# Performance work log

Hardware: AMD Instinct MI355X
Metric: run time of the kernel (lower is better)

Reference implementation:

```python
import jax, jax.numpy as jnp
import numpy as np

NODE = 100000
REL = 2000
E = 600000  # n_edges == triple_size
D = 128
DEPTH = 2
HEADS = 1


def setup_inputs() -> dict:
    key = jax.random.key(0)
    ks = jax.random.split(key, 8)
    features = jax.random.normal(ks[0], (NODE, D), jnp.float32)
    rel_emb = jax.random.normal(ks[1], (REL, D), jnp.float32)
    sp_val = jax.random.uniform(ks[2], (E,), jnp.float32)
    attn_kernels = jax.random.normal(ks[3], (DEPTH, HEADS, 3 * D), jnp.float32) * 0.1
    adj_src = jnp.sort(jax.random.randint(ks[4], (E,), 0, NODE))  # tf.segment_sum needs sorted ids
    adj_dst = jax.random.randint(ks[5], (E,), 0, NODE)
    sp_rel = jax.random.randint(ks[6], (E,), 0, REL)
    sp_row = jnp.arange(E)  # sparse (triple, rel) matrix row indices
    return dict(features=features, rel_emb=rel_emb, sp_val=sp_val,
                attn_kernels=attn_kernels, adj_src=adj_src, adj_dst=adj_dst,
                sp_rel=sp_rel, sp_row=sp_row)


def _segment_softmax(logits, seg, num):
    m = jax.ops.segment_max(logits, seg, num_segments=num)
    e = jnp.exp(logits - m[seg])
    s = jax.ops.segment_sum(e, seg, num_segments=num)
    return e / s[seg]


def reference(features, rel_emb, sp_val, attn_kernels, adj_src, adj_dst, sp_rel, sp_row):
    act = jax.nn.relu
    feats = act(features)
    outputs = [feats]
    for l in range(DEPTH):
        heads = []
        for h in range(HEADS):
            ak = attn_kernels[l, h]  # [3D]
            # sparse (triple x rel) @ rel_emb -> per-edge relation embedding [E, D]
            rels = jax.ops.segment_sum(sp_val[:, None] * rel_emb[sp_rel], sp_row,
                                       num_segments=E)
            # tf.nn.l2_normalize with eps 1e-12
            rels = rels * jax.lax.rsqrt(jnp.maximum(jnp.sum(rels * rels, axis=1,
                                                            keepdims=True), 1e-12))
            neighs = feats[adj_dst]  # [E, D]
            selfs = feats[adj_src]   # [E, D]
            # Householder-style reflection of neighbor features across rels
            proj = jnp.sum(neighs * rels, axis=1, keepdims=True) * rels
            neighs = neighs - 2.0 * proj
            # attention logits: concat([selfs, neighs, rels]) @ ak
            att = selfs @ ak[:D] + neighs @ ak[D:2 * D] + rels @ ak[2 * D:]
            a = _segment_softmax(att, adj_src, NODE)  # tf.sparse_softmax per row
            heads.append(jax.ops.segment_sum(neighs * a[:, None], adj_src,
                                             num_segments=NODE))
        feats = heads[0] if HEADS == 1 else jnp.concatenate(heads, axis=1)
        feats = act(feats)
        outputs.append(feats)
    return jnp.concatenate(outputs, axis=1)  # [NODE, D*(DEPTH+1)]
```

## Files before the change

kernel.cpp:

```cpp
#include <hip/hip_runtime.h>
#include <math.h>
#include <stdint.h>

#define NNODE 100000
#define NREL 2000
#define NEDGE 600000
#define DIM 128
#define OUTC 384
#define LOG2E 1.4426950408889634f

#define RELU_BLOCKS 12500
#define PRE_BLOCKS 500
#define ROW_BLOCKS ((NNODE + 1 + 255) / 256)

typedef float f32x2 __attribute__((ext_vector_type(2)));

__device__ __forceinline__ float wave_sum(float v) {
#pragma unroll
    for (int off = 32; off > 0; off >>= 1)
        v += __shfl_xor(v, off, 64);
    return v;
}

__device__ __forceinline__ float dpp_sum16(float x) {
    x += __int_as_float(__builtin_amdgcn_mov_dpp(__float_as_int(x), 0xB1, 0xF, 0xF, true));
    x += __int_as_float(__builtin_amdgcn_mov_dpp(__float_as_int(x), 0x4E, 0xF, 0xF, true));
    x += __int_as_float(__builtin_amdgcn_mov_dpp(__float_as_int(x), 0x124, 0xF, 0xF, true));
    x += __int_as_float(__builtin_amdgcn_mov_dpp(__float_as_int(x), 0x128, 0xF, 0xF, true));
    return x;
}

__device__ __forceinline__ unsigned short f2bf(float f) {
    unsigned b = __float_as_uint(f);
    return (unsigned short)((b + 0x7fffu + ((b >> 16) & 1u)) >> 16);
}
__device__ __forceinline__ unsigned pack2(float f0, float f1) {
    return (unsigned)f2bf(f0) | ((unsigned)f2bf(f1) << 16);
}
__device__ __forceinline__ f32x2 bf2(unsigned u) {
    f32x2 r;
    r.x = __uint_as_float(u << 16);
    r.y = __uint_as_float(u & 0xffff0000u);
    return r;
}

__global__ void k_setup(const float* __restrict__ f, const float* __restrict__ rel,
                        const float* __restrict__ attn, const int* __restrict__ adj_src,
                        float* __restrict__ out, unsigned short* __restrict__ fm,
                        unsigned short* __restrict__ relm,
                        float* __restrict__ relnorm2, float* __restrict__ rdB,
                        float* __restrict__ rdC,
                        float* __restrict__ nd0, int* __restrict__ row_ptr) {
    int b = blockIdx.x;
    if (b < RELU_BLOCKS) {
        int idx = b * 256 + threadIdx.x;
        int n = idx >> 5;
        int q = idx & 31;
        float4 v = reinterpret_cast<const float4*>(f + (size_t)n * DIM)[q];
        v.x = fmaxf(v.x, 0.f); v.y = fmaxf(v.y, 0.f);
        v.z = fmaxf(v.z, 0.f); v.w = fmaxf(v.w, 0.f);
        reinterpret_cast<float4*>(out + (size_t)n * OUTC)[q] = v;
        uint2 p;
        p.x = pack2(v.x, v.y);
        p.y = pack2(v.z, v.w);
        reinterpret_cast<uint2*>(fm + (size_t)n * DIM)[q] = p;
        float4 bb = reinterpret_cast<const float4*>(attn + DIM)[q];
        float pb = v.x * bb.x + v.y * bb.y + v.z * bb.z + v.w * bb.w;
#pragma unroll
        for (int off = 1; off <= 16; off <<= 1)
            pb += __shfl_xor(pb, off, 64);
        if (q == 0) nd0[n] = pb * LOG2E;
    } else if (b < RELU_BLOCKS + PRE_BLOCKS) {
        int wid = (b - RELU_BLOCKS) * 4 + (threadIdx.x >> 6);
        int lane = threadIdx.x & 63;
        float2 v = reinterpret_cast<const float2*>(rel + (size_t)wid * DIM)[lane];
        reinterpret_cast<unsigned*>(relm + (size_t)wid * DIM)[lane] = pack2(v.x, v.y);
        float2 b0 = reinterpret_cast<const float2*>(attn + DIM)[lane];
        float2 c0 = reinterpret_cast<const float2*>(attn + 2 * DIM)[lane];
        float2 b1 = reinterpret_cast<const float2*>(attn + 3 * DIM + DIM)[lane];
        float2 c1 = reinterpret_cast<const float2*>(attn + 3 * DIM + 2 * DIM)[lane];
        float n2  = wave_sum(v.x * v.x + v.y * v.y);
        float pb0 = wave_sum(v.x * b0.x + v.y * b0.y);
        float pc0 = wave_sum(v.x * c0.x + v.y * c0.y);
        float pb1 = wave_sum(v.x * b1.x + v.y * b1.y);
        float pc1 = wave_sum(v.x * c1.x + v.y * c1.y);
        if (lane == 0) {
            relnorm2[wid] = n2;
            rdB[wid] = pb0;        rdC[wid] = pc0;
            rdB[NREL + wid] = pb1; rdC[NREL + wid] = pc1;
        }
    } else {
        int n = (b - RELU_BLOCKS - PRE_BLOCKS) * 256 + threadIdx.x;
        if (n <= NNODE) {
            int lo = 0, hi = NEDGE;
            while (lo < hi) {
                int mid = (lo + hi) >> 1;
                if (adj_src[mid] < n) lo = mid + 1; else hi = mid;
            }
            row_ptr[n] = lo;
        }
    }
}

__global__ void k_edges(const float* __restrict__ sp_val, const int* __restrict__ sp_rel,
                        const int* __restrict__ adj_dst,
                        const float* __restrict__ relnorm2,
                        const float* __restrict__ rdB, const float* __restrict__ rdC,
                        const float* __restrict__ nd0,
                        float4* __restrict__ ed0, float4* __restrict__ ed1) {
    int e = blockIdx.x * blockDim.x + threadIdx.x;
    if (e >= NEDGE) return;
    float v = sp_val[e];
    int r = sp_rel[e];
    int dst = adj_dst[e];
    float n2 = relnorm2[r];
    float sc = v * rsqrtf(fmaxf(v * v * n2, 1e-12f));
    float q2 = 2.f * sc * sc;
    float scl = sc * LOG2E, q2l = q2 * LOG2E;
    unsigned pk = ((unsigned)dst << 11) | (unsigned)r;
    float pkf = __uint_as_float(pk);
    ed0[e] = make_float4(nd0[dst] + scl * rdC[r], q2l * rdB[r], q2, pkf);
    ed1[e] = make_float4(scl * rdC[NREL + r], q2l * rdB[NREL + r], q2, pkf);
}

__global__ void k_fold(float4* __restrict__ ed, const float* __restrict__ nd) {
    int e = blockIdx.x * blockDim.x + threadIdx.x;
    if (e >= NEDGE) return;
    float4 v = ed[e];
    unsigned pk = __float_as_uint(v.w);
    ed[e].x = v.x + nd[pk >> 11];
}

template<int USE_ED, int WRITE_NEXT>
__global__ __launch_bounds__(256, 8)
void k_gat(const unsigned short* __restrict__ fin_m,
           float* __restrict__ fout,
           unsigned short* __restrict__ fout_m,
           const unsigned short* __restrict__ relm,
           const float4* __restrict__ edata,
           const int* __restrict__ adj_dst, const int* __restrict__ sp_rel,
           const float* __restrict__ sp_val, const float* __restrict__ relnorm2,
           const float* __restrict__ rdB, const float* __restrict__ rdC,
           const float* __restrict__ ndpre,
           const int* __restrict__ row_ptr,
           float* __restrict__ nd_n,
           const float* __restrict__ akB_next) {
    int wv = (blockIdx.x * blockDim.x + threadIdx.x) >> 6;
    int lane = threadIdx.x & 63;
    int g = lane >> 4, gl = lane & 15;
    int node = wv * 4 + g;
    if (node >= NNODE) return;
    int e0 = row_ptr[node], e1 = row_ptr[node + 1];

    f32x2 acc0 = 0.f, acc1 = 0.f, acc2 = 0.f, acc3 = 0.f;
    float s = 0.f;

    auto ld = [&](int ee, uint4& fb_, uint4& rb_, float& ab_, float& qb_, float& q2_) {
        fb_ = make_uint4(0, 0, 0, 0); rb_ = make_uint4(0, 0, 0, 0);
        ab_ = 0.f; qb_ = 0.f; q2_ = 0.f;
        if (ee < e1) {
            int dst, r;
            if (USE_ED) {
                float4 ed = edata[ee];
                unsigned pk = __float_as_uint(ed.w);
                dst = (int)(pk >> 11); r = (int)(pk & 2047u);
                ab_ = ed.x; qb_ = ed.y; q2_ = ed.z;
            } else {
                dst = adj_dst[ee]; r = sp_rel[ee];
                float v = sp_val[ee];
                float sc = v * rsqrtf(fmaxf(v * v * relnorm2[r], 1e-12f));
                q2_ = 2.f * sc * sc;
                qb_ = q2_ * LOG2E * rdB[r];
                ab_ = ndpre[dst] + sc * LOG2E * rdC[r];
            }
            fb_ = *reinterpret_cast<const uint4*>(fin_m + (unsigned)((dst << 7) + (gl << 3)));
            rb_ = *reinterpret_cast<const uint4*>(relm + (unsigned)((r << 7) + (gl << 3)));
        }
    };

    uint4 fbA, rbA, fbB, rbB;
    float abA, qbA, q2A, abB, qbB, q2B;
    int e = e0;
    ld(e, fbA, rbA, abA, qbA, q2A);
    ld(e + 1, fbB, rbB, abB, qbB, q2B);
    while (e < e1) {
        uint4 fbC, rbC;
        float abC, qbC, q2C;
        ld(e + 2, fbC, rbC, abC, qbC, q2C);

        f32x2 f0 = bf2(fbA.x), f1 = bf2(fbA.y), f2 = bf2(fbA.z), f3 = bf2(fbA.w);
        f32x2 r0 = bf2(rbA.x), r1 = bf2(rbA.y), r2 = bf2(rbA.z), r3 = bf2(rbA.w);
        f32x2 d2 = f0 * r0;
        d2 += f1 * r1;
        d2 += f2 * r2;
        d2 += f3 * r3;
        float dot = dpp_sum16(d2.x + d2.y);
        float w = __builtin_exp2f(abA - dot * qbA);
        float k2 = dot * q2A;
        s += w;
        acc0 += w * (f0 - k2 * r0);
        acc1 += w * (f1 - k2 * r1);
        acc2 += w * (f2 - k2 * r2);
        acc3 += w * (f3 - k2 * r3);

        fbA = fbB; rbA = rbB; abA = abB; qbA = qbB; q2A = q2B;
        fbB = fbC; rbB = rbC; abB = abC; qbB = qbC; q2B = q2C;
        ++e;
    }

    float inv = (s > 0.f) ? 1.f / s : 0.f;
    float o[8];
    o[0] = fmaxf(acc0.x * inv, 0.f); o[1] = fmaxf(acc0.y * inv, 0.f);
    o[2] = fmaxf(acc1.x * inv, 0.f); o[3] = fmaxf(acc1.y * inv, 0.f);
    o[4] = fmaxf(acc2.x * inv, 0.f); o[5] = fmaxf(acc2.y * inv, 0.f);
    o[6] = fmaxf(acc3.x * inv, 0.f); o[7] = fmaxf(acc3.y * inv, 0.f);
    float4* op = reinterpret_cast<float4*>(fout + (unsigned)(node * OUTC + gl * 8));
    op[0] = make_float4(o[0], o[1], o[2], o[3]);
    op[1] = make_float4(o[4], o[5], o[6], o[7]);
    if (WRITE_NEXT) {
        uint4 mw;
        mw.x = pack2(o[0], o[1]); mw.y = pack2(o[2], o[3]);
        mw.z = pack2(o[4], o[5]); mw.w = pack2(o[6], o[7]);
        *reinterpret_cast<uint4*>(fout_m + (unsigned)((node << 7) + (gl << 3))) = mw;
        const float4* aB = reinterpret_cast<const float4*>(akB_next) + gl * 2;
        float4 b0 = aB[0], b1 = aB[1];
        float pb = o[0] * b0.x + o[1] * b0.y + o[2] * b0.z + o[3] * b0.w
                 + o[4] * b1.x + o[5] * b1.y + o[6] * b1.z + o[7] * b1.w;
        pb = dpp_sum16(pb);
        if (gl == 0) nd_n[node] = pb * LOG2E;
    }
}

extern "C" void kernel_launch(void* const* d_in, const int* in_sizes, int n_in,
                              void* d_out, int out_size, void* d_ws, size_t ws_size,
                              hipStream_t stream) {
    const float* features = (const float*)d_in[0];
    const float* rel_emb  = (const float*)d_in[1];
    const float* sp_val   = (const float*)d_in[2];
    const float* attn     = (const float*)d_in[3];
    const int*   adj_src  = (const int*)d_in[4];
    const int*   adj_dst  = (const int*)d_in[5];
    const int*   sp_rel   = (const int*)d_in[6];
    float* out = (float*)d_out;

    char* p = (char*)d_ws;
    unsigned short* mir0 = (unsigned short*)p; p += (size_t)NNODE * DIM * 2;
    unsigned short* mir1 = (unsigned short*)p; p += (size_t)NNODE * DIM * 2;
    unsigned short* relm = (unsigned short*)p; p += (size_t)NREL * DIM * 2;
    float* nd0      = (float*)p; p += (size_t)NNODE * 4;
    float* nd1      = (float*)p; p += (size_t)NNODE * 4;
    float* relnorm2 = (float*)p; p += (size_t)NREL * 4;
    float* rdB      = (float*)p; p += (size_t)2 * NREL * 4;
    float* rdC      = (float*)p; p += (size_t)2 * NREL * 4;
    int*   row_ptr  = (int*)p;   p += (size_t)(NNODE + 1) * 4;
    p = (char*)(((uintptr_t)p + 15) & ~(uintptr_t)15);
    float4* ed0 = (float4*)p; p += (size_t)NEDGE * 16;
    float4* ed1 = (float4*)p; p += (size_t)NEDGE * 16;
    size_t needed = (size_t)(p - (char*)d_ws);
    bool use_ed = (ws_size >= needed);

    k_setup<<<RELU_BLOCKS + PRE_BLOCKS + ROW_BLOCKS, 256, 0, stream>>>(
        features, rel_emb, attn, adj_src, out, mir0, relm,
        relnorm2, rdB, rdC, nd0, row_ptr);

    int gat_blocks = (NNODE / 4 * 64) / 256;
    const float* akB1 = attn + 3 * DIM + DIM;

    if (use_ed) {
        k_edges<<<(NEDGE + 255) / 256, 256, 0, stream>>>(
            sp_val, sp_rel, adj_dst, relnorm2, rdB, rdC, nd0, ed0, ed1);
        k_gat<1, 1><<<gat_blocks, 256, 0, stream>>>(
            mir0, out + DIM, mir1, relm, ed0, adj_dst, sp_rel, sp_val, relnorm2,
            rdB, rdC, nd0, row_ptr, nd1, akB1);
        k_fold<<<(NEDGE + 255) / 256, 256, 0, stream>>>(ed1, nd1);
        k_gat<1, 0><<<gat_blocks, 256, 0, stream>>>(
            mir1, out + 2 * DIM, (unsigned short*)nullptr, relm, ed1, adj_dst, sp_rel,
            sp_val, relnorm2, rdB + NREL, rdC + NREL, nd1, row_ptr,
            (float*)nullptr, (const float*)nullptr);
    } else {
        k_gat<0, 1><<<gat_blocks, 256, 0, stream>>>(
            mir0, out + DIM, mir1, relm, (const float4*)nullptr, adj_dst, sp_rel,
            sp_val, relnorm2, rdB, rdC, nd0, row_ptr, nd1, akB1);
        k_gat<0, 0><<<gat_blocks, 256, 0, stream>>>(
            mir1, out + 2 * DIM, (unsigned short*)nullptr, relm, (const float4*)nullptr,
            adj_dst, sp_rel, sp_val, relnorm2, rdB + NREL, rdC + NREL, nd1, row_ptr,
            (float*)nullptr, (const float*)nullptr);
    }
}
```

Measured before the change: 140.2 us.

## Sort nodes by degree for load-balanced GAT wave scheduling

Builds a degree histogram in the setup kernel, scans it, and writes a permutation that groups nodes with similar degree. The GAT kernels process nodes through this permutation, so the four 16-lane groups in a wave see similar edge counts and less work is lost to divergence. It also drops the launch-bounds occupancy hint from k_gat. The cost is an extra memset, a scan launch, a second binary search per node, and an indirect node lookup that scatters output writes.

```diff
diff --git a/kernel.cpp b/kernel.cpp
--- a/kernel.cpp
+++ b/kernel.cpp
@@ -12,6 +12,8 @@
 #define RELU_BLOCKS 12500
 #define PRE_BLOCKS 500
 #define ROW_BLOCKS ((NNODE + 1 + 255) / 256)
+#define EDGE_BLOCKS ((NEDGE + 255) / 256)
+#define PERM_BLOCKS ((NNODE + 255) / 256)
 
 typedef float f32x2 __attribute__((ext_vector_type(2)));
 
@@ -50,7 +52,8 @@
                         unsigned short* __restrict__ relm,
                         float* __restrict__ relnorm2, float* __restrict__ rdB,
                         float* __restrict__ rdC,
-                        float* __restrict__ nd0, int* __restrict__ row_ptr) {
+                        float* __restrict__ nd0, int* __restrict__ row_ptr,
+                        int* __restrict__ hist) {
     int b = blockIdx.x;
     if (b < RELU_BLOCKS) {
         int idx = b * 256 + threadIdx.x;
@@ -98,8 +101,30 @@
                 if (adj_src[mid] < n) lo = mid + 1; else hi = mid;
             }
             row_ptr[n] = lo;
+            if (n < NNODE) {
+                int n1 = n + 1;
+                int lo2 = lo, hi2 = NEDGE;
+                while (lo2 < hi2) {
+                    int mid = (lo2 + hi2) >> 1;
+                    if (adj_src[mid] < n1) lo2 = mid + 1; else hi2 = mid;
+                }
+                int bin = min(lo2 - lo, 63);
+                atomicAdd(&hist[bin], 1);
+            }
         }
     }
+}
+
+__global__ void k_scan(const int* __restrict__ hist, int* __restrict__ binpos) {
+    int lane = threadIdx.x;
+    int v = hist[lane];
+    int inc = v;
+#pragma unroll
+    for (int off = 1; off < 64; off <<= 1) {
+        int o = __shfl_up(inc, off, 64);
+        if (lane >= off) inc += o;
+    }
+    binpos[lane] = inc - v;
 }
 
 __global__ void k_edges(const float* __restrict__ sp_val, const int* __restrict__ sp_rel,
@@ -107,20 +132,43 @@
                         const float* __restrict__ relnorm2,
                         const float* __restrict__ rdB, const float* __restrict__ rdC,
                         const float* __restrict__ nd0,
-                        float4* __restrict__ ed0, float4* __restrict__ ed1) {
-    int e = blockIdx.x * blockDim.x + threadIdx.x;
-    if (e >= NEDGE) return;
-    float v = sp_val[e];
-    int r = sp_rel[e];
-    int dst = adj_dst[e];
-    float n2 = relnorm2[r];
-    float sc = v * rsqrtf(fmaxf(v * v * n2, 1e-12f));
-    float q2 = 2.f * sc * sc;
-    float scl = sc * LOG2E, q2l = q2 * LOG2E;
-    unsigned pk = ((unsigned)dst << 11) | (unsigned)r;
-    float pkf = __uint_as_float(pk);
-    ed0[e] = make_float4(nd0[dst] + scl * rdC[r], q2l * rdB[r], q2, pkf);
-    ed1[e] = make_float4(scl * rdC[NREL + r], q2l * rdB[NREL + r], q2, pkf);
+                        float4* __restrict__ ed0, float4* __restrict__ ed1,
+                        const int* __restrict__ row_ptr, int* __restrict__ binpos,
+                        int* __restrict__ perm) {
+    __shared__ int lh[64];
+    __shared__ int lbase[64];
+    int b = blockIdx.x;
+    if (b < EDGE_BLOCKS) {
+        int e = b * 256 + threadIdx.x;
+        if (e >= NEDGE) return;
+        float v = sp_val[e];
+        int r = sp_rel[e];
+        int dst = adj_dst[e];
+        float n2 = relnorm2[r];
+        float sc = v * rsqrtf(fmaxf(v * v * n2, 1e-12f));
+        float q2 = 2.f * sc * sc;
+        float scl = sc * LOG2E, q2l = q2 * LOG2E;
+        unsigned pk = ((unsigned)dst << 11) | (unsigned)r;
+        float pkf = __uint_as_float(pk);
+        ed0[e] = make_float4(nd0[dst] + scl * rdC[r], q2l * rdB[r], q2, pkf);
+        ed1[e] = make_float4(scl * rdC[NREL + r], q2l * rdB[NREL + r], q2, pkf);
+    } else {
+        int t = threadIdx.x;
+        if (t < 64) lh[t] = 0;
+        __syncthreads();
+        int n = (b - EDGE_BLOCKS) * 256 + t;
+        bool valid = n < NNODE;
+        int bin = 0, myrank = 0;
+        if (valid) {
+            int d = row_ptr[n + 1] - row_ptr[n];
+            bin = min(d, 63);
+            myrank = atomicAdd(&lh[bin], 1);
+        }
+        __syncthreads();
+        if (t < 64 && lh[t] > 0) lbase[t] = atomicAdd(&binpos[t], lh[t]);
+        __syncthreads();
+        if (valid) perm[lbase[bin] + myrank] = n;
+    }
 }
 
 __global__ void k_fold(float4* __restrict__ ed, const float* __restrict__ nd) {
@@ -132,24 +180,25 @@
 }
 
 template<int USE_ED, int WRITE_NEXT>
-__global__ __launch_bounds__(256, 8)
-void k_gat(const unsigned short* __restrict__ fin_m,
-           float* __restrict__ fout,
-           unsigned short* __restrict__ fout_m,
-           const unsigned short* __restrict__ relm,
-           const float4* __restrict__ edata,
-           const int* __restrict__ adj_dst, const int* __restrict__ sp_rel,
-           const float* __restrict__ sp_val, const float* __restrict__ relnorm2,
-           const float* __restrict__ rdB, const float* __restrict__ rdC,
-           const float* __restrict__ ndpre,
-           const int* __restrict__ row_ptr,
-           float* __restrict__ nd_n,
-           const float* __restrict__ akB_next) {
+__global__ void k_gat(const unsigned short* __restrict__ fin_m,
+                      float* __restrict__ fout,
+                      unsigned short* __restrict__ fout_m,
+                      const unsigned short* __restrict__ relm,
+                      const float4* __restrict__ edata,
+                      const int* __restrict__ adj_dst, const int* __restrict__ sp_rel,
+                      const float* __restrict__ sp_val, const float* __restrict__ relnorm2,
+                      const float* __restrict__ rdB, const float* __restrict__ rdC,
+                      const float* __restrict__ ndpre,
+                      const int* __restrict__ row_ptr,
+                      const int* __restrict__ perm,
+                      float* __restrict__ nd_n,
+                      const float* __restrict__ akB_next) {
     int wv = (blockIdx.x * blockDim.x + threadIdx.x) >> 6;
     int lane = threadIdx.x & 63;
     int g = lane >> 4, gl = lane & 15;
-    int node = wv * 4 + g;
-    if (node >= NNODE) return;
+    int idx = wv * 4 + g;
+    if (idx >= NNODE) return;
+    int node = perm[idx];
     int e0 = row_ptr[node], e1 = row_ptr[node + 1];
 
     f32x2 acc0 = 0.f, acc1 = 0.f, acc2 = 0.f, acc3 = 0.f;
@@ -253,37 +302,46 @@
     float* rdB      = (float*)p; p += (size_t)2 * NREL * 4;
     float* rdC      = (float*)p; p += (size_t)2 * NREL * 4;
     int*   row_ptr  = (int*)p;   p += (size_t)(NNODE + 1) * 4;
+    int*   hist     = (int*)p;   p += 64 * 4;
+    int*   binpos   = (int*)p;   p += 64 * 4;
+    int*   perm     = (int*)p;   p += (size_t)NNODE * 4;
     p = (char*)(((uintptr_t)p + 15) & ~(uintptr_t)15);
     float4* ed0 = (float4*)p; p += (size_t)NEDGE * 16;
     float4* ed1 = (float4*)p; p += (size_t)NEDGE * 16;
     size_t needed = (size_t)(p - (char*)d_ws);
     bool use_ed = (ws_size >= needed);
 
+    hipMemsetAsync(hist, 0, 64 * sizeof(int), stream);
+
     k_setup<<<RELU_BLOCKS + PRE_BLOCKS + ROW_BLOCKS, 256, 0, stream>>>(
         features, rel_emb, attn, adj_src, out, mir0, relm,
-        relnorm2, rdB, rdC, nd0, row_ptr);
+        relnorm2, rdB, rdC, nd0, row_ptr, hist);
+
+    k_scan<<<1, 64, 0, stream>>>(hist, binpos);
+
+    k_edges<<<EDGE_BLOCKS + PERM_BLOCKS, 256, 0, stream>>>(
+        sp_val, sp_rel, adj_dst, relnorm2, rdB, rdC, nd0, ed0, ed1,
+        row_ptr, binpos, perm);
 
     int gat_blocks = (NNODE / 4 * 64) / 256;
     const float* akB1 = attn + 3 * DIM + DIM;
 
     if (use_ed) {
-        k_edges<<<(NEDGE + 255) / 256, 256, 0, stream>>>(
-            sp_val, sp_rel, adj_dst, relnorm2, rdB, rdC, nd0, ed0, ed1);
         k_gat<1, 1><<<gat_blocks, 256, 0, stream>>>(
             mir0, out + DIM, mir1, relm, ed0, adj_dst, sp_rel, sp_val, relnorm2,
-            rdB, rdC, nd0, row_ptr, nd1, akB1);
+            rdB, rdC, nd0, row_ptr, perm, nd1, akB1);
         k_fold<<<(NEDGE + 255) / 256, 256, 0, stream>>>(ed1, nd1);
         k_gat<1, 0><<<gat_blocks, 256, 0, stream>>>(
             mir1, out + 2 * DIM, (unsigned short*)nullptr, relm, ed1, adj_dst, sp_rel,
-            sp_val, relnorm2, rdB + NREL, rdC + NREL, nd1, row_ptr,
+            sp_val, relnorm2, rdB + NREL, rdC + NREL, nd1, row_ptr, perm,
             (float*)nullptr, (const float*)nullptr);
     } else {
         k_gat<0, 1><<<gat_blocks, 256, 0, stream>>>(
             mir0, out + DIM, mir1, relm, (const float4*)nullptr, adj_dst, sp_rel,
-            sp_val, relnorm2, rdB, rdC, nd0, row_ptr, nd1, akB1);
+            sp_val, relnorm2, rdB, rdC, nd0, row_ptr, perm, nd1, akB1);
         k_gat<0, 0><<<gat_blocks, 256, 0, stream>>>(
             mir1, out + 2 * DIM, (unsigned short*)nullptr, relm, (const float4*)nullptr,
-            adj_dst, sp_rel, sp_val, relnorm2, rdB + NREL, rdC + NREL, nd1, row_ptr,
+            adj_dst, sp_rel, sp_val, relnorm2, rdB + NREL, rdC + NREL, nd1, row_ptr, perm,
             (float*)nullptr, (const float*)nullptr);
     }
 }
```

New measurement: 515.8 us. 268% more time.

## Process each node with a full wave, splitting edges across quarter-waves

Applied to the files above, without the earlier changes.

The GAT aggregation kernel now assigns one 64-lane wave per node instead of four nodes per wave. Each 16-lane group takes every fourth edge, and the partial sums are merged with cross-lane shuffles before group 0 writes the output. This is meant to cut serial edge-loop length and raise memory-level parallelism for high-degree nodes. The separate k_fold pass is removed and the per-node term is added inside the second-layer load instead. The cost is four times as many waves, idle lanes on low-degree nodes, and extra shuffle reductions.

```diff
diff --git a/kernel.cpp b/kernel.cpp
--- a/kernel.cpp
+++ b/kernel.cpp
@@ -123,33 +123,23 @@
     ed1[e] = make_float4(scl * rdC[NREL + r], q2l * rdB[NREL + r], q2, pkf);
 }
 
-__global__ void k_fold(float4* __restrict__ ed, const float* __restrict__ nd) {
-    int e = blockIdx.x * blockDim.x + threadIdx.x;
-    if (e >= NEDGE) return;
-    float4 v = ed[e];
-    unsigned pk = __float_as_uint(v.w);
-    ed[e].x = v.x + nd[pk >> 11];
-}
-
-template<int USE_ED, int WRITE_NEXT>
-__global__ __launch_bounds__(256, 8)
-void k_gat(const unsigned short* __restrict__ fin_m,
-           float* __restrict__ fout,
-           unsigned short* __restrict__ fout_m,
-           const unsigned short* __restrict__ relm,
-           const float4* __restrict__ edata,
-           const int* __restrict__ adj_dst, const int* __restrict__ sp_rel,
-           const float* __restrict__ sp_val, const float* __restrict__ relnorm2,
-           const float* __restrict__ rdB, const float* __restrict__ rdC,
-           const float* __restrict__ ndpre,
-           const int* __restrict__ row_ptr,
-           float* __restrict__ nd_n,
-           const float* __restrict__ akB_next) {
-    int wv = (blockIdx.x * blockDim.x + threadIdx.x) >> 6;
+template<int USE_ED, int NDIN, int WRITE_NEXT>
+__global__ void k_gat(const unsigned short* __restrict__ fin_m,
+                      float* __restrict__ fout,
+                      unsigned short* __restrict__ fout_m,
+                      const unsigned short* __restrict__ relm,
+                      const float4* __restrict__ edata,
+                      const int* __restrict__ adj_dst, const int* __restrict__ sp_rel,
+                      const float* __restrict__ sp_val, const float* __restrict__ relnorm2,
+                      const float* __restrict__ rdB, const float* __restrict__ rdC,
+                      const float* __restrict__ ndpre,
+                      const int* __restrict__ row_ptr,
+                      float* __restrict__ nd_n,
+                      const float* __restrict__ akB_next) {
+    int node = (blockIdx.x * blockDim.x + threadIdx.x) >> 6;
     int lane = threadIdx.x & 63;
+    if (node >= NNODE) return;
     int g = lane >> 4, gl = lane & 15;
-    int node = wv * 4 + g;
-    if (node >= NNODE) return;
     int e0 = row_ptr[node], e1 = row_ptr[node + 1];
 
     f32x2 acc0 = 0.f, acc1 = 0.f, acc2 = 0.f, acc3 = 0.f;
@@ -164,7 +154,8 @@
                 float4 ed = edata[ee];
                 unsigned pk = __float_as_uint(ed.w);
                 dst = (int)(pk >> 11); r = (int)(pk & 2047u);
-                ab_ = ed.x; qb_ = ed.y; q2_ = ed.z;
+                ab_ = NDIN ? ed.x + ndpre[dst] : ed.x;
+                qb_ = ed.y; q2_ = ed.z;
             } else {
                 dst = adj_dst[ee]; r = sp_rel[ee];
                 float v = sp_val[ee];
@@ -180,13 +171,13 @@
 
     uint4 fbA, rbA, fbB, rbB;
     float abA, qbA, q2A, abB, qbB, q2B;
-    int e = e0;
+    int e = e0 + g;
     ld(e, fbA, rbA, abA, qbA, q2A);
-    ld(e + 1, fbB, rbB, abB, qbB, q2B);
+    ld(e + 4, fbB, rbB, abB, qbB, q2B);
     while (e < e1) {
         uint4 fbC, rbC;
         float abC, qbC, q2C;
-        ld(e + 2, fbC, rbC, abC, qbC, q2C);
+        ld(e + 8, fbC, rbC, abC, qbC, q2C);
 
         f32x2 f0 = bf2(fbA.x), f1 = bf2(fbA.y), f2 = bf2(fbA.z), f3 = bf2(fbA.w);
         f32x2 r0 = bf2(rbA.x), r1 = bf2(rbA.y), r2 = bf2(rbA.z), r3 = bf2(rbA.w);
@@ -195,7 +186,7 @@
         d2 += f2 * r2;
         d2 += f3 * r3;
         float dot = dpp_sum16(d2.x + d2.y);
-        float w = __builtin_exp2f(abA - dot * qbA);
+        float w = (e < e1) ? __builtin_exp2f(abA - dot * qbA) : 0.f;
         float k2 = dot * q2A;
         s += w;
         acc0 += w * (f0 - k2 * r0);
@@ -205,29 +196,42 @@
 
         fbA = fbB; rbA = rbB; abA = abB; qbA = qbB; q2A = q2B;
         fbB = fbC; rbB = rbC; abB = abC; qbB = qbC; q2B = q2C;
-        ++e;
-    }
-
-    float inv = (s > 0.f) ? 1.f / s : 0.f;
-    float o[8];
-    o[0] = fmaxf(acc0.x * inv, 0.f); o[1] = fmaxf(acc0.y * inv, 0.f);
-    o[2] = fmaxf(acc1.x * inv, 0.f); o[3] = fmaxf(acc1.y * inv, 0.f);
-    o[4] = fmaxf(acc2.x * inv, 0.f); o[5] = fmaxf(acc2.y * inv, 0.f);
-    o[6] = fmaxf(acc3.x * inv, 0.f); o[7] = fmaxf(acc3.y * inv, 0.f);
-    float4* op = reinterpret_cast<float4*>(fout + (unsigned)(node * OUTC + gl * 8));
-    op[0] = make_float4(o[0], o[1], o[2], o[3]);
-    op[1] = make_float4(o[4], o[5], o[6], o[7]);
-    if (WRITE_NEXT) {
-        uint4 mw;
-        mw.x = pack2(o[0], o[1]); mw.y = pack2(o[2], o[3]);
-        mw.z = pack2(o[4], o[5]); mw.w = pack2(o[6], o[7]);
-        *reinterpret_cast<uint4*>(fout_m + (unsigned)((node << 7) + (gl << 3))) = mw;
-        const float4* aB = reinterpret_cast<const float4*>(akB_next) + gl * 2;
-        float4 b0 = aB[0], b1 = aB[1];
-        float pb = o[0] * b0.x + o[1] * b0.y + o[2] * b0.z + o[3] * b0.w
-                 + o[4] * b1.x + o[5] * b1.y + o[6] * b1.z + o[7] * b1.w;
-        pb = dpp_sum16(pb);
-        if (gl == 0) nd_n[node] = pb * LOG2E;
+        e += 4;
+    }
+
+    auto mrg = [](float v) {
+        v += __shfl_xor(v, 16, 64);
+        v += __shfl_xor(v, 32, 64);
+        return v;
+    };
+    s = mrg(s);
+    acc0.x = mrg(acc0.x); acc0.y = mrg(acc0.y);
+    acc1.x = mrg(acc1.x); acc1.y = mrg(acc1.y);
+    acc2.x = mrg(acc2.x); acc2.y = mrg(acc2.y);
+    acc3.x = mrg(acc3.x); acc3.y = mrg(acc3.y);
+
+    if (g == 0) {
+        float inv = (s > 0.f) ? 1.f / s : 0.f;
+        float o[8];
+        o[0] = fmaxf(acc0.x * inv, 0.f); o[1] = fmaxf(acc0.y * inv, 0.f);
+        o[2] = fmaxf(acc1.x * inv, 0.f); o[3] = fmaxf(acc1.y * inv, 0.f);
+        o[4] = fmaxf(acc2.x * inv, 0.f); o[5] = fmaxf(acc2.y * inv, 0.f);
+        o[6] = fmaxf(acc3.x * inv, 0.f); o[7] = fmaxf(acc3.y * inv, 0.f);
+        float4* op = reinterpret_cast<float4*>(fout + (unsigned)(node * OUTC + gl * 8));
+        op[0] = make_float4(o[0], o[1], o[2], o[3]);
+        op[1] = make_float4(o[4], o[5], o[6], o[7]);
+        if (WRITE_NEXT) {
+            uint4 mw;
+            mw.x = pack2(o[0], o[1]); mw.y = pack2(o[2], o[3]);
+            mw.z = pack2(o[4], o[5]); mw.w = pack2(o[6], o[7]);
+            *reinterpret_cast<uint4*>(fout_m + (unsigned)((node << 7) + (gl << 3))) = mw;
+            const float4* aB = reinterpret_cast<const float4*>(akB_next) + gl * 2;
+            float4 b0 = aB[0], b1 = aB[1];
+            float pb = o[0] * b0.x + o[1] * b0.y + o[2] * b0.z + o[3] * b0.w
+                     + o[4] * b1.x + o[5] * b1.y + o[6] * b1.z + o[7] * b1.w;
+            pb = dpp_sum16(pb);
+            if (gl == 0) nd_n[node] = pb * LOG2E;
+        }
     }
 }
 
@@ -263,25 +267,24 @@
         features, rel_emb, attn, adj_src, out, mir0, relm,
         relnorm2, rdB, rdC, nd0, row_ptr);
 
-    int gat_blocks = (NNODE / 4 * 64) / 256;
+    int gat_blocks = (NNODE * 64) / 256;
     const float* akB1 = attn + 3 * DIM + DIM;
 
     if (use_ed) {
         k_edges<<<(NEDGE + 255) / 256, 256, 0, stream>>>(
             sp_val, sp_rel, adj_dst, relnorm2, rdB, rdC, nd0, ed0, ed1);
-        k_gat<1, 1><<<gat_blocks, 256, 0, stream>>>(
+        k_gat<1, 0, 1><<<gat_blocks, 256, 0, stream>>>(
             mir0, out + DIM, mir1, relm, ed0, adj_dst, sp_rel, sp_val, relnorm2,
             rdB, rdC, nd0, row_ptr, nd1, akB1);
-        k_fold<<<(NEDGE + 255) / 256, 256, 0, stream>>>(ed1, nd1);
-        k_gat<1, 0><<<gat_blocks, 256, 0, stream>>>(
+        k_gat<1, 1, 0><<<gat_blocks, 256, 0, stream>>>(
             mir1, out + 2 * DIM, (unsigned short*)nullptr, relm, ed1, adj_dst, sp_rel,
             sp_val, relnorm2, rdB + NREL, rdC + NREL, nd1, row_ptr,
             (float*)nullptr, (const float*)nullptr);
     } else {
-        k_gat<0, 1><<<gat_blocks, 256, 0, stream>>>(
+        k_gat<0, 1, 1><<<gat_blocks, 256, 0, stream>>>(
             mir0, out + DIM, mir1, relm, (const float4*)nullptr, adj_dst, sp_rel,
             sp_val, relnorm2, rdB, rdC, nd0, row_ptr, nd1, akB1);
-        k_gat<0, 0><<<gat_blocks, 256, 0, stream>>>(
+        k_gat<0, 1, 0><<<gat_blocks, 256, 0, stream>>>(
             mir1, out + 2 * DIM, (unsigned short*)nullptr, relm, (const float4*)nullptr,
             adj_dst, sp_rel, sp_val, relnorm2, rdB + NREL, rdC + NREL, nd1, row_ptr,
             (float*)nullptr, (const float*)nullptr);
```

Result: slower. 146.1 us (+4.3%).
